# Optimization experiments

Hardware: AMD Instinct MI355X
Metric: run time of the kernel (lower is better)

## Reference

```python
import jax, jax.numpy as jnp
import numpy as np

C_IN = 128
C_HID = 32   # per-head hidden dim (passed to Attention as c_hidden)
N_HEADS = 4
N = 384      # I == J (required by triangle bias broadcast)
INF = 1000000000.0
LN_EPS = 1e-5


def setup_inputs() -> dict:
    key = jax.random.key(0)
    ks = jax.random.split(key, 12)
    hc = N_HEADS * C_HID
    s_in = 1.0 / np.sqrt(C_IN)
    s_hc = 1.0 / np.sqrt(hc)
    return {
        "x": jax.random.normal(ks[0], (N, N, C_IN), jnp.float32),
        "mask": jnp.ones((N, N), jnp.float32),
        "ln_g": jnp.ones((C_IN,), jnp.float32),
        "ln_b": jnp.zeros((C_IN,), jnp.float32),
        "w_tri": jax.random.normal(ks[1], (C_IN, N_HEADS), jnp.float32) * s_in,
        "wq": jax.random.normal(ks[2], (C_IN, hc), jnp.float32) * s_in,
        "wk": jax.random.normal(ks[3], (C_IN, hc), jnp.float32) * s_in,
        "wv": jax.random.normal(ks[4], (C_IN, hc), jnp.float32) * s_in,
        "wg": jax.random.normal(ks[5], (C_IN, hc), jnp.float32) * s_in,
        "bg": jnp.ones((hc,), jnp.float32),
        "wo": jax.random.normal(ks[6], (hc, C_IN), jnp.float32) * s_hc,
        "bo": jnp.zeros((C_IN,), jnp.float32),
    }


def reference(x, mask, ln_g, ln_b, w_tri, wq, wk, wv, wg, bg, wo, bo):
    I, J, C = x.shape
    H = w_tri.shape[1]
    ch = wq.shape[1] // H

    # LayerNorm over channel dim
    mu = jnp.mean(x, axis=-1, keepdims=True)
    var = jnp.mean((x - mu) ** 2, axis=-1, keepdims=True)
    xn = (x - mu) * jax.lax.rsqrt(var + LN_EPS) * ln_g + ln_b

    # Biases
    mask_bias = INF * (mask - 1.0)          # [I, J] -> broadcast [I,1,1,J]
    tri = xn @ w_tri                         # [I, J, H]
    tri_bias = jnp.transpose(tri, (2, 0, 1))[None]  # [1, H, I(q), J(k)]

    # Per-row multi-head attention over J
    q = (xn @ wq).reshape(I, J, H, ch)
    k = (xn @ wk).reshape(I, J, H, ch)
    v = (xn @ wv).reshape(I, J, H, ch)
    scale = 1.0 / np.sqrt(ch)

    scores = jnp.einsum("iqhc,ikhc->ihqk", q, k) * scale  # [I,H,J,J]
    scores = scores + mask_bias[:, None, None, :] + tri_bias
    a = jax.nn.softmax(scores, axis=-1)

    o = jnp.einsum("ihqk,ikhc->iqhc", a, v).reshape(I, J, H * ch)
    g = jax.nn.sigmoid(xn @ wg + bg)
    return (o * g) @ wo + bo  # [I, J, C]
```

## Files before the change

kernel.cpp:

```cpp
#include <hip/hip_runtime.h>

#define DEVFN __device__ __forceinline__

typedef short bf16x8 __attribute__((ext_vector_type(8)));
typedef float f32x4 __attribute__((ext_vector_type(4)));
typedef float f32x16 __attribute__((ext_vector_type(16)));

constexpr int NN = 384;
constexpr int MROWS = NN * NN;
constexpr float LN_EPS = 1e-5f;
constexpr float INFB = 1000000000.0f;
constexpr float LOG2E = 1.44269504088896340736f;
constexpr float SM_SCALE = 0.17677669529663687f;

DEVFN unsigned short f2bf(float f) {
  unsigned u = __builtin_bit_cast(unsigned, f);
  u += 0x7fffu + ((u >> 16) & 1u);
  return (unsigned short)(u >> 16);
}
DEVFN float bflo(unsigned u) { return __builtin_bit_cast(float, u << 16); }
DEVFN float bfhi(unsigned u) { return __builtin_bit_cast(float, u & 0xffff0000u); }
DEVFN unsigned cvtpk(float lo, float hi) {
  unsigned d;
  asm("v_cvt_pk_bf16_f32 %0, %1, %2" : "=v"(d) : "v"(lo), "v"(hi));
  return d;
}
DEVFN void swap32(unsigned &a, unsigned &b) {
  asm volatile("v_permlane32_swap_b32 %0, %1" : "+v"(a), "+v"(b));
}
DEVFN void gload16(const void* g, void* l) {
  __builtin_amdgcn_global_load_lds((const __attribute__((address_space(1))) void*)g,
                                   (__attribute__((address_space(3))) void*)l, 16, 0, 0);
}

__global__ __launch_bounds__(256) void k_ln(
    const float* __restrict__ x, const float* __restrict__ ln_g,
    const float* __restrict__ ln_b, const float* __restrict__ w_tri,
    unsigned* __restrict__ xn2, unsigned short* __restrict__ trib) {
  const int lane = threadIdx.x & 63;
  const int wid = blockIdx.x * 4 + (threadIdx.x >> 6);
  const int nw = gridDim.x * 4;
  const float g0 = ln_g[2*lane], g1 = ln_g[2*lane+1];
  const float b0 = ln_b[2*lane], b1 = ln_b[2*lane+1];
  float wt[8];
#pragma unroll
  for (int h = 0; h < 4; ++h) { wt[h] = w_tri[(2*lane)*4 + h]; wt[4+h] = w_tri[(2*lane+1)*4 + h]; }
  for (int row = wid; row < MROWS; row += nw) {
    const float2 v = *(const float2*)(x + (size_t)row*128 + 2*lane);
    float s = v.x + v.y, sq = v.x*v.x + v.y*v.y;
#pragma unroll
    for (int o = 1; o < 64; o <<= 1) { s += __shfl_xor(s, o, 64); sq += __shfl_xor(sq, o, 64); }
    const float mu = s * 0.0078125f;
    const float rs = rsqrtf(sq * 0.0078125f - mu*mu + LN_EPS);
    const float xn0 = (v.x - mu)*rs*g0 + b0;
    const float xn1 = (v.y - mu)*rs*g1 + b1;
    xn2[(size_t)row*64 + lane] = cvtpk(xn0, xn1);
    float t0 = xn0*wt[0] + xn1*wt[4];
    float t1 = xn0*wt[1] + xn1*wt[5];
    float t2 = xn0*wt[2] + xn1*wt[6];
    float t3 = xn0*wt[3] + xn1*wt[7];
#pragma unroll
    for (int o = 1; o < 64; o <<= 1) {
      t0 += __shfl_xor(t0, o, 64); t1 += __shfl_xor(t1, o, 64);
      t2 += __shfl_xor(t2, o, 64); t3 += __shfl_xor(t3, o, 64);
    }
    if (lane < 4) {
      const float tv = lane==0?t0 : lane==1?t1 : lane==2?t2 : t3;
      const int i = row / NN, j = row - i*NN;
      trib[(((size_t)lane*12 + (j>>5))*NN + i)*32 + (j&31)] = f2bf(tv);
    }
  }
}

__global__ __launch_bounds__(256) void k_proj(
    const unsigned short* __restrict__ xn, const unsigned short* __restrict__ Wt,
    const float* __restrict__ bg,
    unsigned short* __restrict__ Qb, unsigned short* __restrict__ Kb,
    unsigned short* __restrict__ VTb, unsigned short* __restrict__ Gb) {
  __shared__ __align__(16) char lds[49152];
  const int tid = threadIdx.x;
  const int lane = tid & 63, w = tid >> 6;
  const int nb = blockIdx.x & 3, mt = blockIdx.x >> 2;
  const int m00 = mt * 64;
  const int l15 = lane & 15, l4 = lane >> 4;
  const char* Ag = (const char*)xn + (size_t)m00 * 256;
#pragma unroll
  for (int c = 0; c < 4; ++c) {
    const int fa = w*4 + c;
    gload16(Ag + ((fa>>2)*16 + l15)*256 + (fa&3)*64 + l4*16, lds + fa*1024);
  }
  const char* Bg = (const char*)Wt + (size_t)nb * 128 * 256;
#pragma unroll
  for (int c = 0; c < 8; ++c) {
    const int fb = w*8 + c;
    gload16(Bg + ((fb>>2)*16 + l15)*256 + (fb&3)*64 + l4*16, lds + 16384 + fb*1024);
  }
  __syncthreads();
  const int wm = w >> 1, wn = w & 1;
  f32x4 acc[2][4] = {};
#pragma unroll
  for (int kk = 0; kk < 4; ++kk) {
    bf16x8 a[2], b[4];
#pragma unroll
    for (int mi = 0; mi < 2; ++mi)
      a[mi] = *(const bf16x8*)(lds + ((wm*2+mi)*4 + kk)*1024 + lane*16);
#pragma unroll
    for (int ni = 0; ni < 4; ++ni)
      b[ni] = *(const bf16x8*)(lds + 16384 + ((wn*4+ni)*4 + kk)*1024 + lane*16);
#pragma unroll
    for (int mi = 0; mi < 2; ++mi)
#pragma unroll
      for (int ni = 0; ni < 4; ++ni)
        acc[mi][ni] = __builtin_amdgcn_mfma_f32_16x16x32_bf16(a[mi], b[ni], acc[mi][ni], 0, 0, 0);
  }
  const int i0 = m00 / NN;
  const int j0 = m00 - i0*NN;
  if (nb != 2) {
    unsigned short* dst = nb==0 ? Qb : (nb==1 ? Kb : Gb);
    float bgv[4] = {0.f,0.f,0.f,0.f};
    if (nb == 3) {
#pragma unroll
      for (int ni = 0; ni < 4; ++ni) bgv[ni] = bg[wn*64 + ni*16 + l15];
    }
#pragma unroll
    for (int mi = 0; mi < 2; ++mi)
#pragma unroll
      for (int ni = 0; ni < 4; ++ni) {
        const int n = wn*64 + ni*16 + l15;
#pragma unroll
        for (int r = 0; r < 4; ++r) {
          const int j = j0 + wm*32 + mi*16 + l4*4 + r;
          float v = acc[mi][ni][r];
          if (nb == 3) v = 1.f / (1.f + exp2f(-(v + bgv[ni]) * LOG2E));
          dst[(((size_t)(i0*4 + (n>>5))*NN) + j)*32 + (n&31)] = f2bf(v);
        }
      }
  } else {
    __syncthreads();
    float* T = (float*)lds;
#pragma unroll
    for (int mi = 0; mi < 2; ++mi)
#pragma unroll
      for (int ni = 0; ni < 4; ++ni) {
        const int n = wn*64 + ni*16 + l15;
#pragma unroll
        for (int r = 0; r < 4; ++r)
          T[n*65 + wm*32 + mi*16 + l4*4 + r] = acc[mi][ni][r];
      }
    __syncthreads();
#pragma unroll
    for (int it = 0; it < 4; ++it) {
      const int slot = it*256 + tid;
      const int n = slot >> 3, j8 = (slot & 7)*8;
      const float* src = T + n*65 + j8;
      uint4 pk;
      pk.x = cvtpk(src[0], src[1]); pk.y = cvtpk(src[2], src[3]);
      pk.z = cvtpk(src[4], src[5]); pk.w = cvtpk(src[6], src[7]);
      *(uint4*)((char*)VTb + ((((size_t)(i0*4 + (n>>5))*32) + (n&31))*NN + j0 + j8)*2) = pk;
    }
  }
}

__global__ __launch_bounds__(256) void k_attn(
    const unsigned short* __restrict__ Qb, const unsigned short* __restrict__ Kb,
    const unsigned short* __restrict__ VTb, const unsigned short* __restrict__ trib,
    const float* __restrict__ mask,
    const unsigned short* Gb, unsigned short* opre) {
  __shared__ __align__(16) char lds[50688];
  const int tid = threadIdx.x;
  const int lane = tid & 63, w = tid >> 6;
  const int i = blockIdx.x >> 2, h = blockIdx.x & 3;
  const int lo = lane & 31, hi = lane >> 5;
  const size_t ih = (size_t)(i*4 + h);
  const char* Kg = (const char*)Kb + ih * 384 * 64;
  const char* Vg = (const char*)VTb + ih * 32 * 768;
#pragma unroll
  for (int c = 0; c < 6; ++c) {
    const int fk = w*6 + c;
    gload16(Kg + ((fk>>1)*32 + lo)*64 + (fk&1)*32 + hi*16, lds + fk*1024);
  }
#pragma unroll
  for (int c = 0; c < 6; ++c) {
    const int fv = w*6 + c;
    gload16(Vg + lo*768 + fv*32 + hi*16, lds + 24576 + fv*1024);
  }
  float* mb = (float*)(lds + 49152);
  for (int j = tid; j < 384; j += 256) mb[j] = INFB * (mask[i*384 + j] - 1.f);
  __syncthreads();
  const char* Qg = (const char*)Qb + ih * 384 * 64;
  for (int it = 0; it < 3; ++it) {
    const int qg = (it*4 + w)*32 + lo;
    bf16x8 qf[2];
    qf[0] = *(const bf16x8*)(Qg + qg*64 + hi*16);
    qf[1] = *(const bf16x8*)(Qg + qg*64 + 32 + hi*16);
    f32x16 O;
#pragma unroll
    for (int r = 0; r < 16; ++r) O[r] = 0.f;
    float m_r = -1e30f, l_r = 0.f;
    for (int kt = 0; kt < 12; ++kt) {
      f32x16 st;
#pragma unroll
      for (int r = 0; r < 16; ++r) st[r] = 0.f;
#pragma unroll
      for (int dc = 0; dc < 2; ++dc) {
        const bf16x8 ka = *(const bf16x8*)(lds + (kt*2+dc)*1024 + lane*16);
        st = __builtin_amdgcn_mfma_f32_32x32x16_bf16(ka, qf[dc], st, 0, 0, 0);
      }
      const char* trow = (const char*)trib + (((size_t)(h*12 + kt)*384 + qg)*32)*2;
      float s[16];
#pragma unroll
      for (int rr = 0; rr < 4; ++rr) {
        const uint2 tv = *(const uint2*)(trow + (8*rr + 4*hi)*2);
        const float4 mv = *(const float4*)(mb + kt*32 + 8*rr + 4*hi);
        s[rr*4+0] = st[rr*4+0]*SM_SCALE + bflo(tv.x) + mv.x;
        s[rr*4+1] = st[rr*4+1]*SM_SCALE + bfhi(tv.x) + mv.y;
        s[rr*4+2] = st[rr*4+2]*SM_SCALE + bflo(tv.y) + mv.z;
        s[rr*4+3] = st[rr*4+3]*SM_SCALE + bfhi(tv.y) + mv.w;
      }
      float pmax = s[0];
#pragma unroll
      for (int r = 1; r < 16; ++r) pmax = fmaxf(pmax, s[r]);
      pmax = fmaxf(pmax, __shfl_xor(pmax, 32, 64));
      const float mnew = fmaxf(m_r, pmax);
      const float fs = exp2f((m_r - mnew) * LOG2E);
      float p[16], psum = 0.f;
#pragma unroll
      for (int r = 0; r < 16; ++r) { p[r] = exp2f((s[r] - mnew) * LOG2E); psum += p[r]; }
      psum += __shfl_xor(psum, 32, 64);
      l_r = l_r * fs + psum;
      m_r = mnew;
#pragma unroll
      for (int r = 0; r < 16; ++r) O[r] *= fs;
      unsigned w0 = cvtpk(p[0], p[1]),   w1 = cvtpk(p[2], p[3]);
      unsigned w2 = cvtpk(p[4], p[5]),   w3 = cvtpk(p[6], p[7]);
      unsigned w4 = cvtpk(p[8], p[9]),   w5 = cvtpk(p[10], p[11]);
      unsigned w6 = cvtpk(p[12], p[13]), w7 = cvtpk(p[14], p[15]);
      swap32(w0, w2); swap32(w1, w3); swap32(w4, w6); swap32(w5, w7);
      union { unsigned u[4]; bf16x8 v; } pa, pb;
      pa.u[0] = w0; pa.u[1] = w1; pa.u[2] = w2; pa.u[3] = w3;
      pb.u[0] = w4; pb.u[1] = w5; pb.u[2] = w6; pb.u[3] = w7;
      const bf16x8 va = *(const bf16x8*)(lds + 24576 + (kt*2)*1024 + lane*16);
      O = __builtin_amdgcn_mfma_f32_32x32x16_bf16(va, pa.v, O, 0, 0, 0);
      const bf16x8 vb = *(const bf16x8*)(lds + 24576 + (kt*2+1)*1024 + lane*16);
      O = __builtin_amdgcn_mfma_f32_32x32x16_bf16(vb, pb.v, O, 0, 0, 0);
    }
    const float rl = 1.f / l_r;
    const char* grow = (const char*)Gb + (ih*384 + qg)*64;
    char* orow = (char*)opre + (ih*384 + qg)*64;
#pragma unroll
    for (int rr = 0; rr < 4; ++rr) {
      const uint2 gv = *(const uint2*)(grow + (8*rr + 4*hi)*2);
      uint2 ov;
      ov.x = cvtpk(O[rr*4+0]*rl*bflo(gv.x), O[rr*4+1]*rl*bfhi(gv.x));
      ov.y = cvtpk(O[rr*4+2]*rl*bflo(gv.y), O[rr*4+3]*rl*bfhi(gv.y));
      *(uint2*)(orow + (8*rr + 4*hi)*2) = ov;
    }
  }
}

__global__ __launch_bounds__(256) void k_out(
    const unsigned short* __restrict__ opre, const unsigned short* __restrict__ woT,
    const float* __restrict__ bo, float* __restrict__ out) {
  __shared__ __align__(16) char lds[32768];
  const int tid = threadIdx.x;
  const int lane = tid & 63, w = tid >> 6;
  const int m00 = blockIdx.x * 64;
  const int l15 = lane & 15, l4 = lane >> 4;
#pragma unroll
  for (int c = 0; c < 8; ++c) {
    const int fb = w*8 + c;
    gload16((const char*)woT + ((fb>>2)*16 + l15)*256 + (fb&3)*64 + l4*16, lds + fb*1024);
  }
  __syncthreads();
  const int wm = w >> 1, wn = w & 1;
  const int i0 = m00 / NN, j0 = m00 - i0*NN;
  f32x4 acc[2][4] = {};
#pragma unroll
  for (int kk = 0; kk < 4; ++kk) {
    bf16x8 a[2], b[4];
#pragma unroll
    for (int mi = 0; mi < 2; ++mi) {
      const int j = j0 + wm*32 + mi*16 + l15;
      a[mi] = *(const bf16x8*)((const char*)opre + ((size_t)(i0*4 + kk)*NN + j)*64 + l4*16);
    }
#pragma unroll
    for (int ni = 0; ni < 4; ++ni)
      b[ni] = *(const bf16x8*)(lds + ((wn*4+ni)*4 + kk)*1024 + lane*16);
#pragma unroll
    for (int mi = 0; mi < 2; ++mi)
#pragma unroll
      for (int ni = 0; ni < 4; ++ni)
        acc[mi][ni] = __builtin_amdgcn_mfma_f32_16x16x32_bf16(a[mi], b[ni], acc[mi][ni], 0, 0, 0);
  }
  float bov[4];
#pragma unroll
  for (int ni = 0; ni < 4; ++ni) bov[ni] = bo[wn*64 + ni*16 + l15];
#pragma unroll
  for (int mi = 0; mi < 2; ++mi)
#pragma unroll
    for (int ni = 0; ni < 4; ++ni) {
      const int n = wn*64 + ni*16 + l15;
#pragma unroll
      for (int r = 0; r < 4; ++r) {
        const int j = j0 + wm*32 + mi*16 + l4*4 + r;
        out[((size_t)i0*NN + j)*128 + n] = acc[mi][ni][r] + bov[ni];
      }
    }
}

__global__ __launch_bounds__(256) void k_pack(
    const float* __restrict__ wq, const float* __restrict__ wk,
    const float* __restrict__ wv, const float* __restrict__ wg,
    const float* __restrict__ wo,
    unsigned short* __restrict__ Wt, unsigned short* __restrict__ woT) {
  const int stride = gridDim.x * 256;
  for (int o = blockIdx.x*256 + threadIdx.x; o < 81920; o += stride) {
    if (o < 65536) {
      const int row = o >> 7, k = o & 127;
      const int s = row >> 7, n = row & 127;
      const float* W = s==0 ? wq : s==1 ? wk : s==2 ? wv : wg;
      Wt[o] = f2bf(W[k*128 + n]);
    } else {
      const int o2 = o - 65536;
      const int n = o2 >> 7, k = o2 & 127;
      woT[o2] = f2bf(wo[k*128 + n]);
    }
  }
}

extern "C" void kernel_launch(void* const* d_in, const int* in_sizes, int n_in,
                              void* d_out, int out_size, void* d_ws, size_t ws_size,
                              hipStream_t stream) {
  const float* x     = (const float*)d_in[0];
  const float* mask  = (const float*)d_in[1];
  const float* ln_g  = (const float*)d_in[2];
  const float* ln_b  = (const float*)d_in[3];
  const float* w_tri = (const float*)d_in[4];
  const float* wq    = (const float*)d_in[5];
  const float* wk    = (const float*)d_in[6];
  const float* wv    = (const float*)d_in[7];
  const float* wg    = (const float*)d_in[8];
  const float* bg    = (const float*)d_in[9];
  const float* wo    = (const float*)d_in[10];
  const float* bo    = (const float*)d_in[11];
  float* outp = (float*)d_out;
  (void)in_sizes; (void)n_in; (void)out_size; (void)ws_size;

  char* ws = (char*)d_ws;
  size_t off = 0;
  auto carve = [&](size_t b) { char* p = ws + off; off += (b + 255) & ~(size_t)255; return p; };
  const size_t big = (size_t)MROWS * 256;
  unsigned short* xn   = (unsigned short*)carve(big);
  unsigned short* Qb   = (unsigned short*)carve(big);
  unsigned short* Kb   = (unsigned short*)carve(big);
  unsigned short* VTb  = (unsigned short*)carve(big);
  unsigned short* Gb   = (unsigned short*)carve(big);
  unsigned short* trib = (unsigned short*)carve((size_t)4*12*384*32*2);
  unsigned short* Wt   = (unsigned short*)carve(512*128*2);
  unsigned short* woT  = (unsigned short*)carve(128*128*2);

  k_pack<<<96, 256, 0, stream>>>(wq, wk, wv, wg, wo, Wt, woT);
  k_ln<<<1024, 256, 0, stream>>>(x, ln_g, ln_b, w_tri, (unsigned*)xn, trib);
  k_proj<<<9216, 256, 0, stream>>>(xn, Wt, bg, Qb, Kb, VTb, Gb);
  k_attn<<<1536, 256, 0, stream>>>(Qb, Kb, VTb, trib, mask, Gb, Gb);
  k_out<<<2304, 256, 0, stream>>>(Gb, woT, bo, outp);
}
```

Baseline: 417.9 us.

## Fold softmax scale and log2e into weights and biases, preload bias into MFMA accumulator

Folds the 1/sqrt(d)·log2(e) factor into the packed Q weight, log2(e) into w_tri and the mask bias, so scores arrive already in the exp2 domain. The triangle and mask bias are loaded into the MFMA accumulator before the QK^T product instead of being added afterwards, which removes per-element multiplies and adds in the softmax loop. It also adds a launch_bounds occupancy hint of 4 blocks. Rounding Q to bf16 after scaling slightly changes numerics.

```diff
diff --git a/kernel.cpp b/kernel.cpp
--- a/kernel.cpp
+++ b/kernel.cpp
@@ -12,6 +12,7 @@
 constexpr float INFB = 1000000000.0f;
 constexpr float LOG2E = 1.44269504088896340736f;
 constexpr float SM_SCALE = 0.17677669529663687f;
+constexpr float QSCALE = SM_SCALE * LOG2E;
 
 DEVFN unsigned short f2bf(float f) {
   unsigned u = __builtin_bit_cast(unsigned, f);
@@ -44,7 +45,10 @@
   const float b0 = ln_b[2*lane], b1 = ln_b[2*lane+1];
   float wt[8];
 #pragma unroll
-  for (int h = 0; h < 4; ++h) { wt[h] = w_tri[(2*lane)*4 + h]; wt[4+h] = w_tri[(2*lane+1)*4 + h]; }
+  for (int h = 0; h < 4; ++h) {
+    wt[h]   = w_tri[(2*lane)*4 + h]   * LOG2E;
+    wt[4+h] = w_tri[(2*lane+1)*4 + h] * LOG2E;
+  }
   for (int row = wid; row < MROWS; row += nw) {
     const float2 v = *(const float2*)(x + (size_t)row*128 + 2*lane);
     float s = v.x + v.y, sq = v.x*v.x + v.y*v.y;
@@ -161,7 +165,7 @@
   }
 }
 
-__global__ __launch_bounds__(256) void k_attn(
+__global__ __launch_bounds__(256, 4) void k_attn(
     const unsigned short* __restrict__ Qb, const unsigned short* __restrict__ Kb,
     const unsigned short* __restrict__ VTb, const unsigned short* __restrict__ trib,
     const float* __restrict__ mask,
@@ -185,7 +189,7 @@
     gload16(Vg + lo*768 + fv*32 + hi*16, lds + 24576 + fv*1024);
   }
   float* mb = (float*)(lds + 49152);
-  for (int j = tid; j < 384; j += 256) mb[j] = INFB * (mask[i*384 + j] - 1.f);
+  for (int j = tid; j < 384; j += 256) mb[j] = (INFB * LOG2E) * (mask[i*384 + j] - 1.f);
   __syncthreads();
   const char* Qg = (const char*)Qb + ih * 384 * 64;
   for (int it = 0; it < 3; ++it) {
@@ -198,34 +202,32 @@
     for (int r = 0; r < 16; ++r) O[r] = 0.f;
     float m_r = -1e30f, l_r = 0.f;
     for (int kt = 0; kt < 12; ++kt) {
+      const char* trow = (const char*)trib + (((size_t)(h*12 + kt)*384 + qg)*32)*2;
       f32x16 st;
 #pragma unroll
-      for (int r = 0; r < 16; ++r) st[r] = 0.f;
+      for (int rr = 0; rr < 4; ++rr) {
+        const int kb = 8*rr + 4*hi;
+        const uint2 tv = *(const uint2*)(trow + kb*2);
+        const float4 mv = *(const float4*)(mb + kt*32 + kb);
+        st[rr*4+0] = bflo(tv.x) + mv.x;
+        st[rr*4+1] = bfhi(tv.x) + mv.y;
+        st[rr*4+2] = bflo(tv.y) + mv.z;
+        st[rr*4+3] = bfhi(tv.y) + mv.w;
+      }
 #pragma unroll
       for (int dc = 0; dc < 2; ++dc) {
         const bf16x8 ka = *(const bf16x8*)(lds + (kt*2+dc)*1024 + lane*16);
         st = __builtin_amdgcn_mfma_f32_32x32x16_bf16(ka, qf[dc], st, 0, 0, 0);
       }
-      const char* trow = (const char*)trib + (((size_t)(h*12 + kt)*384 + qg)*32)*2;
-      float s[16];
-#pragma unroll
-      for (int rr = 0; rr < 4; ++rr) {
-        const uint2 tv = *(const uint2*)(trow + (8*rr + 4*hi)*2);
-        const float4 mv = *(const float4*)(mb + kt*32 + 8*rr + 4*hi);
-        s[rr*4+0] = st[rr*4+0]*SM_SCALE + bflo(tv.x) + mv.x;
-        s[rr*4+1] = st[rr*4+1]*SM_SCALE + bfhi(tv.x) + mv.y;
-        s[rr*4+2] = st[rr*4+2]*SM_SCALE + bflo(tv.y) + mv.z;
-        s[rr*4+3] = st[rr*4+3]*SM_SCALE + bfhi(tv.y) + mv.w;
-      }
-      float pmax = s[0];
-#pragma unroll
-      for (int r = 1; r < 16; ++r) pmax = fmaxf(pmax, s[r]);
+      float pmax = st[0];
+#pragma unroll
+      for (int r = 1; r < 16; ++r) pmax = fmaxf(pmax, st[r]);
       pmax = fmaxf(pmax, __shfl_xor(pmax, 32, 64));
       const float mnew = fmaxf(m_r, pmax);
-      const float fs = exp2f((m_r - mnew) * LOG2E);
+      const float fs = exp2f(m_r - mnew);
       float p[16], psum = 0.f;
 #pragma unroll
-      for (int r = 0; r < 16; ++r) { p[r] = exp2f((s[r] - mnew) * LOG2E); psum += p[r]; }
+      for (int r = 0; r < 16; ++r) { p[r] = exp2f(st[r] - mnew); psum += p[r]; }
       psum += __shfl_xor(psum, 32, 64);
       l_r = l_r * fs + psum;
       m_r = mnew;
@@ -319,7 +321,8 @@
       const int row = o >> 7, k = o & 127;
       const int s = row >> 7, n = row & 127;
       const float* W = s==0 ? wq : s==1 ? wk : s==2 ? wv : wg;
-      Wt[o] = f2bf(W[k*128 + n]);
+      const float sc = (s == 0) ? QSCALE : 1.f;
+      Wt[o] = f2bf(W[k*128 + n] * sc);
     } else {
       const int o2 = o - 65536;
       const int n = o2 >> 7, k = o2 & 127;
```

After: 419.2 us. Within noise of the previous version (+0.3%).
